# Kernel tuning notes

Measured on AMD Instinct MI355X. Metric: run time of the kernel, lower is better.

## Reference

```python
import jax, jax.numpy as jnp
import numpy as np

N = 4096      # nodes
F = 512       # nfeat
D = 64        # nhid per head
H = 8         # nheads
C = 40        # nclass
ALPHA = 0.2   # leakyrelu slope
NEG = -1e9    # mask value (finite for bf16/fp16 safety; exp -> 0)
EDGE_P = 0.004


def setup_inputs() -> dict:
    key = jax.random.key(0)
    ks = jax.random.split(key, 8)
    x = jax.random.normal(ks[0], (N, F), jnp.float32)
    adj = jax.random.uniform(ks[1], (N, N)) < EDGE_P
    adj = adj | jnp.eye(N, dtype=bool)  # self-loops: every softmax row valid
    init = lambda k, shape, fan: jax.random.normal(k, shape, jnp.float32) / np.sqrt(fan)
    W1 = init(ks[2], (H, F, D), F)        # per-head tran.weight^T
    a1_src = init(ks[3], (H, D), D)       # att1 (j / source term)
    a1_dst = init(ks[4], (H, D), D)       # att2 (i / destination term)
    W2 = init(ks[5], (H * D, C), H * D)   # output head tran
    a2_src = init(ks[6], (C,), C)
    a2_dst = init(ks[7], (C,), C)
    return dict(x=x, adj=adj, W1=W1, a1_src=a1_src, a1_dst=a1_dst,
                W2=W2, a2_src=a2_src, a2_dst=a2_dst)


def reference(x, adj, W1, a1_src, a1_dst, W2, a2_src, a2_dst):
    # ---- layer 1: H heads in parallel (dropout = identity in eval) ----
    h = jnp.einsum('nf,hfd->hnd', x, W1)              # [H,N,D]
    si = jnp.einsum('hnd,hd->hn', h, a1_dst)          # att2(h): i term
    sj = jnp.einsum('hnd,hd->hn', h, a1_src)          # att1(h): j term
    e = jax.nn.leaky_relu(si[:, :, None] + sj[:, None, :], ALPHA)  # [H,N,N]
    e = jnp.where(adj[None], e, NEG)                  # mask non-edges
    p = jax.nn.softmax(e, axis=-1)                    # softmax over neighbors j
    out = jnp.einsum('hij,hjd->hid', p, h)            # [H,N,D]
    # torch.cat(heads, dim=1) -> [N, H*D] with heads contiguous
    x2 = jax.nn.elu(jnp.transpose(out, (1, 0, 2)).reshape(N, H * D))
    # ---- output attention head ----
    h2 = x2 @ W2                                      # [N,C]
    e2 = jax.nn.leaky_relu((h2 @ a2_dst)[:, None] + (h2 @ a2_src)[None, :], ALPHA)
    e2 = jnp.where(adj, e2, NEG)
    p2 = jax.nn.softmax(e2, axis=-1)
    return p2 @ h2                                    # [N,C]
```

## Files before the change

### kernel.cpp

```cpp
#include <hip/hip_runtime.h>

#define NN 4096
#define FF 512
#define DD 64
#define HH 8
#define CC 40
#define HD (HH * DD)
#define CP 64
#define MAXDEG 128
#define ALPHA 0.2f

#define L2BM 8
#define L2BK 32

typedef __attribute__((ext_vector_type(8))) short bf16x8;
typedef __attribute__((ext_vector_type(4))) float f32x4;

__device__ __forceinline__ float bf2f(unsigned short u) {
    union { unsigned int i; float f; } v;
    v.i = ((unsigned int)u) << 16;
    return v.f;
}

__device__ __forceinline__ unsigned short f2bf(float f) {
    union { float f; unsigned int u; } v;
    v.f = f;
    unsigned int r = v.u + 0x7fffu + ((v.u >> 16) & 1u);
    return (unsigned short)(r >> 16);
}

__device__ __forceinline__ float wave_sum(float v) {
    #pragma unroll
    for (int off = 32; off; off >>= 1) v += __shfl_xor(v, off, 64);
    return v;
}

__device__ __forceinline__ float wave_max(float v) {
    #pragma unroll
    for (int off = 32; off; off >>= 1) v = fmaxf(v, __shfl_xor(v, off, 64));
    return v;
}

__device__ __forceinline__ float read_f(const void* src, int i, int isBf16) {
    if (isBf16) return bf2f(((const unsigned short*)src)[i]);
    return ((const float*)src)[i];
}

__device__ __forceinline__ int sniff_x(const void* xraw, int tid, int* fS) {
    if (tid == 0) *fS = 1;
    __syncthreads();
    int bad = 0;
    const unsigned int* xw = (const unsigned int*)xraw;
    #pragma unroll
    for (int q = 0; q < 4; q++) {
        unsigned int w = xw[(tid & 255) * 4 + q];
        unsigned int e0 = (w >> 7) & 0xffu;
        unsigned int e1 = (w >> 23) & 0xffu;
        if (e0 >= 0x90u || e1 >= 0x90u) bad = 1;
    }
    if (bad) *fS = 0;
    __syncthreads();
    return *fS;
}

__global__ __launch_bounds__(256) void prep(const unsigned char* __restrict__ adj,
                                            const void* __restrict__ x,
                                            const void* __restrict__ W1,
                                            const void* __restrict__ W2,
                                            const void* __restrict__ a1s,
                                            const void* __restrict__ a1d,
                                            const void* __restrict__ a2s,
                                            const void* __restrict__ a2d,
                                            int* __restrict__ nbr,
                                            int* __restrict__ deg,
                                            unsigned short* __restrict__ W1bth,
                                            unsigned short* __restrict__ W1btl,
                                            float* __restrict__ W2p,
                                            float* __restrict__ a1sf,
                                            float* __restrict__ a1df,
                                            float* __restrict__ a2sf,
                                            float* __restrict__ a2df) {
    __shared__ int cnt;
    __shared__ int fS;
    int t = threadIdx.x;
    int blk = blockIdx.x;

    if (blk < NN) {
        if (t == 0) { cnt = 0; fS = 1; }
        __syncthreads();
        if (adj[(size_t)t * (NN + 1)] == 0) fS = 0;
        __syncthreads();
        int isByte = fS;
        int i = blk;
        if (isByte) {
            uint4 v = ((const uint4*)(adj + (size_t)i * NN))[t];
            unsigned int u[4] = { v.x, v.y, v.z, v.w };
            int base = t * 16;
            #pragma unroll
            for (int q = 0; q < 4; q++) {
                #pragma unroll
                for (int b = 0; b < 4; b++) {
                    if ((u[q] >> (8 * b)) & 0xffu) {
                        int p = atomicAdd(&cnt, 1);
                        if (p < MAXDEG) nbr[(size_t)i * MAXDEG + p] = base + q * 4 + b;
                    }
                }
            }
        } else {
            const int4* row = (const int4*)((const int*)adj + (size_t)i * NN);
            #pragma unroll
            for (int q = 0; q < 4; q++) {
                int idx4 = q * 256 + t;
                int4 v = row[idx4];
                int base = idx4 * 4;
                if (v.x) { int p = atomicAdd(&cnt, 1); if (p < MAXDEG) nbr[(size_t)i * MAXDEG + p] = base; }
                if (v.y) { int p = atomicAdd(&cnt, 1); if (p < MAXDEG) nbr[(size_t)i * MAXDEG + p] = base + 1; }
                if (v.z) { int p = atomicAdd(&cnt, 1); if (p < MAXDEG) nbr[(size_t)i * MAXDEG + p] = base + 2; }
                if (v.w) { int p = atomicAdd(&cnt, 1); if (p < MAXDEG) nbr[(size_t)i * MAXDEG + p] = base + 3; }
            }
        }
        __syncthreads();
        if (t == 0) deg[i] = min(cnt, MAXDEG);
        return;
    }

    int bf = sniff_x(x, t, &fS);

    if (blk < NN + 64) {
        int b = blk - NN;
        int ob = b * 4096 + t * 16;
        int row = ob >> 9;
        int f0 = ob & 511;
        int hd = row >> 6, d = row & 63;
        unsigned short hi[16], lo[16];
        #pragma unroll
        for (int q = 0; q < 16; q++) {
            float v = read_f(W1, (hd * FF + f0 + q) * DD + d, bf);
            unsigned short h16 = f2bf(v);
            hi[q] = h16;
            lo[q] = f2bf(v - bf2f(h16));
        }
        #pragma unroll
        for (int q = 0; q < 16; q++) {
            W1bth[(size_t)row * FF + f0 + q] = hi[q];
            W1btl[(size_t)row * FF + f0 + q] = lo[q];
        }
        return;
    }

    int i = (blk - NN - 64) * 256 + t;
    const int nW2p = HD * CP;
    const int nA1 = HD;
    if (i < nW2p) {
        int k = i / CP, c = i % CP;
        W2p[i] = (c < CC) ? read_f(W2, k * CC + c, bf) : 0.f;
        return;
    }
    i -= nW2p;
    if (i < nA1) { a1sf[i] = read_f(a1s, i, bf); return; }
    i -= nA1;
    if (i < nA1) { a1df[i] = read_f(a1d, i, bf); return; }
    i -= nA1;
    if (i < CC) { a2sf[i] = read_f(a2s, i, bf); return; }
    i -= CC;
    if (i < CC) { a2df[i] = read_f(a2d, i, bf); return; }
}

__global__ __launch_bounds__(256) void l1_gemm(const void* __restrict__ xraw,
                                               const unsigned short* __restrict__ W1bth,
                                               const unsigned short* __restrict__ W1btl,
                                               const float* __restrict__ a1sf,
                                               const float* __restrict__ a1df,
                                               unsigned short* __restrict__ hb,
                                               float* __restrict__ siv,
                                               float* __restrict__ sjv) {
    __shared__ __align__(16) unsigned short AhB[2][64][40];
    __shared__ __align__(16) unsigned short BhB[2][64][40];
    __shared__ int fS;

    int bm = blockIdx.x, hd = blockIdx.y;
    int tid = threadIdx.x;
    int isBf16 = sniff_x(xraw, tid, &fS);

    int wave = tid >> 6, lane = tid & 63;
    int wm = wave >> 1, wn = wave & 1;
    int lr = lane & 15, lg = lane >> 4;
    int srow = tid >> 2;
    int sseg = (tid & 3) * 8;

    const unsigned short* wAp = W1bth + (size_t)(hd * 64 + srow) * FF + sseg;
    const unsigned short* wBp = W1btl + (size_t)(hd * 64 + srow) * FF + sseg;

    f32x4 acc[2][2];
    #pragma unroll
    for (int r = 0; r < 2; r++)
        #pragma unroll
        for (int c = 0; c < 2; c++) acc[r][c] = (f32x4){0.f, 0.f, 0.f, 0.f};

    if (isBf16) {
        const unsigned short* xp = (const unsigned short*)xraw
                                 + (size_t)(bm * 64 + srow) * FF + sseg;
        uint4 ra = *(const uint4*)xp;
        uint4 rb = *(const uint4*)wAp;
        #pragma unroll 4
        for (int kk = 0; kk < FF; kk += 32) {
            int p = (kk >> 5) & 1;
            *(uint4*)&AhB[p][srow][sseg] = ra;
            *(uint4*)&BhB[p][srow][sseg] = rb;
            __syncthreads();
            int kn = (kk + 32 < FF) ? kk + 32 : kk;
            ra = *(const uint4*)(xp + kn);
            rb = *(const uint4*)(wAp + kn);
            bf16x8 a0 = *(const bf16x8*)&AhB[p][wm * 32 + lr][lg * 8];
            bf16x8 a1 = *(const bf16x8*)&AhB[p][wm * 32 + 16 + lr][lg * 8];
            bf16x8 b0 = *(const bf16x8*)&BhB[p][wn * 32 + lr][lg * 8];
            bf16x8 b1 = *(const bf16x8*)&BhB[p][wn * 32 + 16 + lr][lg * 8];
            acc[0][0] = __builtin_amdgcn_mfma_f32_16x16x32_bf16(a0, b0, acc[0][0], 0, 0, 0);
            acc[0][1] = __builtin_amdgcn_mfma_f32_16x16x32_bf16(a0, b1, acc[0][1], 0, 0, 0);
            acc[1][0] = __builtin_amdgcn_mfma_f32_16x16x32_bf16(a1, b0, acc[1][0], 0, 0, 0);
            acc[1][1] = __builtin_amdgcn_mfma_f32_16x16x32_bf16(a1, b1, acc[1][1], 0, 0, 0);
        }
    } else {
        unsigned short (*Ah)[40] = AhB[0];
        unsigned short (*Al)[40] = AhB[1];
        unsigned short (*Bh)[40] = BhB[0];
        unsigned short (*Bl)[40] = BhB[1];
        const float* xp = (const float*)xraw + (size_t)(bm * 64 + srow) * FF + sseg;
        float4 ra0 = *(const float4*)xp;
        float4 ra1 = *(const float4*)(xp + 4);
        uint4 rbh = *(const uint4*)wAp;
        uint4 rbl = *(const uint4*)wBp;
        for (int kk = 0; kk < FF; kk += 32) {
            __syncthreads();
            union { unsigned short s[8]; uint4 v; } uh, ul;
            float fv[8] = { ra0.x, ra0.y, ra0.z, ra0.w, ra1.x, ra1.y, ra1.z, ra1.w };
            #pragma unroll
            for (int q = 0; q < 8; q++) {
                unsigned short h16 = f2bf(fv[q]);
                uh.s[q] = h16;
                ul.s[q] = f2bf(fv[q] - bf2f(h16));
            }
            *(uint4*)&Ah[srow][sseg] = uh.v;
            *(uint4*)&Al[srow][sseg] = ul.v;
            *(uint4*)&Bh[srow][sseg] = rbh;
            *(uint4*)&Bl[srow][sseg] = rbl;
            __syncthreads();
            int kn = (kk + 32 < FF) ? kk + 32 : kk;
            ra0 = *(const float4*)(xp + kn);
            ra1 = *(const float4*)(xp + kn + 4);
            rbh = *(const uint4*)(wAp + kn);
            rbl = *(const uint4*)(wBp + kn);

            bf16x8 a_h0 = *(const bf16x8*)&Ah[wm * 32 + lr][lg * 8];
            bf16x8 a_h1 = *(const bf16x8*)&Ah[wm * 32 + 16 + lr][lg * 8];
            bf16x8 a_l0 = *(const bf16x8*)&Al[wm * 32 + lr][lg * 8];
            bf16x8 a_l1 = *(const bf16x8*)&Al[wm * 32 + 16 + lr][lg * 8];
            bf16x8 b_h0 = *(const bf16x8*)&Bh[wn * 32 + lr][lg * 8];
            bf16x8 b_h1 = *(const bf16x8*)&Bh[wn * 32 + 16 + lr][lg * 8];
            bf16x8 b_l0 = *(const bf16x8*)&Bl[wn * 32 + lr][lg * 8];
            bf16x8 b_l1 = *(const bf16x8*)&Bl[wn * 32 + 16 + lr][lg * 8];

            acc[0][0] = __builtin_amdgcn_mfma_f32_16x16x32_bf16(a_h0, b_h0, acc[0][0], 0, 0, 0);
            acc[0][1] = __builtin_amdgcn_mfma_f32_16x16x32_bf16(a_h0, b_h1, acc[0][1], 0, 0, 0);
            acc[1][0] = __builtin_amdgcn_mfma_f32_16x16x32_bf16(a_h1, b_h0, acc[1][0], 0, 0, 0);
            acc[1][1] = __builtin_amdgcn_mfma_f32_16x16x32_bf16(a_h1, b_h1, acc[1][1], 0, 0, 0);
            acc[0][0] = __builtin_amdgcn_mfma_f32_16x16x32_bf16(a_h0, b_l0, acc[0][0], 0, 0, 0);
            acc[0][1] = __builtin_amdgcn_mfma_f32_16x16x32_bf16(a_h0, b_l1, acc[0][1], 0, 0, 0);
            acc[1][0] = __builtin_amdgcn_mfma_f32_16x16x32_bf16(a_h1, b_l0, acc[1][0], 0, 0, 0);
            acc[1][1] = __builtin_amdgcn_mfma_f32_16x16x32_bf16(a_h1, b_l1, acc[1][1], 0, 0, 0);
            acc[0][0] = __builtin_amdgcn_mfma_f32_16x16x32_bf16(a_l0, b_h0, acc[0][0], 0, 0, 0);
            acc[0][1] = __builtin_amdgcn_mfma_f32_16x16x32_bf16(a_l0, b_h1, acc[0][1], 0, 0, 0);
            acc[1][0] = __builtin_amdgcn_mfma_f32_16x16x32_bf16(a_l1, b_h0, acc[1][0], 0, 0, 0);
            acc[1][1] = __builtin_amdgcn_mfma_f32_16x16x32_bf16(a_l1, b_h1, acc[1][1], 0, 0, 0);
        }
    }

    float adv[2], asv[2];
    #pragma unroll
    for (int fc = 0; fc < 2; fc++) {
        adv[fc] = a1df[hd * DD + wn * 32 + fc * 16 + lr];
        asv[fc] = a1sf[hd * DD + wn * 32 + fc * 16 + lr];
    }
    float pdv[2][4], psv[2][4];
    #pragma unroll
    for (int fr = 0; fr < 2; fr++) {
        #pragma unroll
        for (int q = 0; q < 4; q++) {
            int row = bm * 64 + wm * 32 + fr * 16 + lg * 4 + q;
            int colb = hd * 64 + wn * 32;
            hb[(size_t)row * HD + colb + lr] = f2bf(acc[fr][0][q]);
            hb[(size_t)row * HD + colb + 16 + lr] = f2bf(acc[fr][1][q]);
            float pd = acc[fr][0][q] * adv[0] + acc[fr][1][q] * adv[1];
            float ps = acc[fr][0][q] * asv[0] + acc[fr][1][q] * asv[1];
            #pragma unroll
            for (int off = 1; off < 16; off <<= 1) {
                pd += __shfl_xor(pd, off, 64);
                ps += __shfl_xor(ps, off, 64);
            }
            pdv[fr][q] = pd;
            psv[fr][q] = ps;
        }
    }
    float* sred = (float*)&AhB[0][0][0];
    __syncthreads();
    if (wn == 0 && lr == 0) {
        #pragma unroll
        for (int fr = 0; fr < 2; fr++)
            #pragma unroll
            for (int q = 0; q < 4; q++) {
                int rl = wm * 32 + fr * 16 + lg * 4 + q;
                sred[rl * 2] = pdv[fr][q];
                sred[rl * 2 + 1] = psv[fr][q];
            }
    }
    __syncthreads();
    if (wn == 1 && lr == 0) {
        #pragma unroll
        for (int fr = 0; fr < 2; fr++)
            #pragma unroll
            for (int q = 0; q < 4; q++) {
                int rl = wm * 32 + fr * 16 + lg * 4 + q;
                int row = bm * 64 + rl;
                siv[(size_t)row * HH + hd] = sred[rl * 2] + pdv[fr][q];
                sjv[(size_t)row * HH + hd] = sred[rl * 2 + 1] + psv[fr][q];
            }
    }
}

__global__ __launch_bounds__(256) void l1_attn(const int* __restrict__ nbr,
                                               const int* __restrict__ deg,
                                               const unsigned short* __restrict__ hb,
                                               const float* __restrict__ siv,
                                               const float* __restrict__ sjv,
                                               float* __restrict__ x2) {
    int i = blockIdx.x;
    int tid = threadIdx.x;
    int wave = tid >> 6, lane = tid & 63;
    int d = deg[i];
    __shared__ int js[MAXDEG];
    __shared__ float wls[HH][MAXDEG];
    __shared__ float invs[HH];
    __shared__ __align__(16) float4 red[128];
    for (int k = tid; k < d; k += 256) js[k] = nbr[(size_t)i * MAXDEG + k];
    __syncthreads();

    int hd = wave * 2 + (lane >> 5);
    int l32 = lane & 31;
    float sii = siv[(size_t)i * HH + hd];
    float m = -1e30f;
    for (int k = l32; k < d; k += 32) {
        float sc = sii + sjv[(size_t)js[k] * HH + hd];
        sc = sc > 0.f ? sc : ALPHA * sc;
        wls[hd][k] = sc;
        m = fmaxf(m, sc);
    }
    #pragma unroll
    for (int off = 16; off; off >>= 1) m = fmaxf(m, __shfl_xor(m, off, 64));
    float s = 0.f;
    for (int k = l32; k < d; k += 32) {
        float e = expf(wls[hd][k] - m);
        wls[hd][k] = e;
        s += e;
    }
    #pragma unroll
    for (int off = 16; off; off >>= 1) s += __shfl_xor(s, off, 64);
    if (l32 == 0) invs[hd] = 1.f / fmaxf(s, 1e-30f);
    __syncthreads();

    const uint2* hu2 = (const uint2*)hb;
    int half = tid >> 7;
    int cq = tid & 127;
    const float* wl = wls[cq >> 4];
    float a0 = 0.f, a1 = 0.f, a2 = 0.f, a3 = 0.f;
    int kk = half;
    for (; kk + 4 <= d; kk += 4) {
        uint2 v0 = hu2[(size_t)js[kk] * 128 + cq];
        uint2 v1 = hu2[(size_t)js[kk + 2] * 128 + cq];
        float w0 = wl[kk], w1 = wl[kk + 2];
        a0 = fmaf(w0, bf2f((unsigned short)v0.x), a0);
        a1 = fmaf(w0, bf2f((unsigned short)(v0.x >> 16)), a1);
        a2 = fmaf(w0, bf2f((unsigned short)v0.y), a2);
        a3 = fmaf(w0, bf2f((unsigned short)(v0.y >> 16)), a3);
        a0 = fmaf(w1, bf2f((unsigned short)v1.x), a0);
        a1 = fmaf(w1, bf2f((unsigned short)(v1.x >> 16)), a1);
        a2 = fmaf(w1, bf2f((unsigned short)v1.y), a2);
        a3 = fmaf(w1, bf2f((unsigned short)(v1.y >> 16)), a3);
    }
    for (; kk < d; kk += 2) {
        uint2 v = hu2[(size_t)js[kk] * 128 + cq];
        float w = wl[kk];
        a0 = fmaf(w, bf2f((unsigned short)v.x), a0);
        a1 = fmaf(w, bf2f((unsigned short)(v.x >> 16)), a1);
        a2 = fmaf(w, bf2f((unsigned short)v.y), a2);
        a3 = fmaf(w, bf2f((unsigned short)(v.y >> 16)), a3);
    }
    if (half == 1) red[cq] = make_float4(a0, a1, a2, a3);
    __syncthreads();
    if (half == 0) {
        float4 r = red[cq];
        float inv = invs[cq >> 4];
        a0 = (a0 + r.x) * inv;
        a1 = (a1 + r.y) * inv;
        a2 = (a2 + r.z) * inv;
        a3 = (a3 + r.w) * inv;
        float4 o;
        o.x = a0 > 0.f ? a0 : expm1f(a0);
        o.y = a1 > 0.f ? a1 : expm1f(a1);
        o.z = a2 > 0.f ? a2 : expm1f(a2);
        o.w = a3 > 0.f ? a3 : expm1f(a3);
        *(float4*)(x2 + (size_t)i * HD + cq * 4) = o;
    }
}

__global__ __launch_bounds__(256) void l2_fused(const float* __restrict__ x2,
                                                const float* __restrict__ W2p,
                                                const float* __restrict__ a2sf,
                                                const float* __restrict__ a2df,
                                                float* __restrict__ h2,
                                                float* __restrict__ d1,
                                                float* __restrict__ d2) {
    __shared__ float As[L2BK][L2BM + 1];
    __shared__ float Bs[L2BK][CP + 1];
    int tid = threadIdx.x;
    int bm = blockIdx.x;
    int ar = tid >> 5;
    int ak = tid & 31;
    int br = tid >> 3;
    int bc = (tid & 7) * 8;
    int c = tid & 63;
    int r0 = (tid >> 6) * 2;

    const float* Arow = x2 + (size_t)(bm * L2BM + ar) * FF;

    float acc0 = 0.f, acc1 = 0.f;

    float av = Arow[ak];
    float4 bv0 = *(const float4*)(W2p + (size_t)br * CP + bc);
    float4 bv1 = *(const float4*)(W2p + (size_t)br * CP + bc + 4);

    for (int kk = 0; kk < FF; kk += L2BK) {
        __syncthreads();
        As[ak][ar] = av;
        *(float4*)&Bs[br][bc] = bv0;
        *(float4*)&Bs[br][bc + 4] = bv1;
        __syncthreads();
        int kn = (kk + L2BK < FF) ? kk + L2BK : kk;
        av = Arow[kn + ak];
        bv0 = *(const float4*)(W2p + (size_t)(kn + br) * CP + bc);
        bv1 = *(const float4*)(W2p + (size_t)(kn + br) * CP + bc + 4);
        #pragma unroll
        for (int k = 0; k < L2BK; k++) {
            float b = Bs[k][c];
            acc0 = fmaf(As[k][r0], b, acc0);
            acc1 = fmaf(As[k][r0 + 1], b, acc1);
        }
    }

    float accs[2] = { acc0, acc1 };
    float ad = (c < CC) ? a2df[c] : 0.f;
    float as = (c < CC) ? a2sf[c] : 0.f;
    #pragma unroll
    for (int q = 0; q < 2; q++) {
        int row = bm * L2BM + r0 + q;
        if (c < CC) h2[(size_t)row * CC + c] = accs[q];
        float pd = wave_sum(accs[q] * ad);
        float ps = wave_sum(accs[q] * as);
        if (c == 0) { d1[row] = pd; d2[row] = ps; }
    }
}

__global__ __launch_bounds__(256) void l2_attn(const int* __restrict__ nbr,
                                               const int* __restrict__ deg,
                                               const float* __restrict__ h2,
                                               const float* __restrict__ d1,
                                               const float* __restrict__ d2,
                                               float* __restrict__ out) {
    int w = threadIdx.x >> 6, lane = threadIdx.x & 63;
    int i = blockIdx.x * 4 + w;
    int d = deg[i];
    __shared__ int js[4][MAXDEG];
    __shared__ float wls[4][MAXDEG];
    for (int k = lane; k < d; k += 64) js[w][k] = nbr[(size_t)i * MAXDEG + k];

    float sii = d1[i];
    float m = -1e30f;
    for (int k = lane; k < d; k += 64) {
        float sc = sii + d2[js[w][k]];
        sc = sc > 0.f ? sc : ALPHA * sc;
        wls[w][k] = sc;
        m = fmaxf(m, sc);
    }
    m = wave_max(m);
    float s = 0.f;
    for (int k = lane; k < d; k += 64) {
        float e = expf(wls[w][k] - m);
        wls[w][k] = e;
        s += e;
    }
    s = fmaxf(wave_sum(s), 1e-30f);

    int c = lane;
    if (c < CC) {
        float acc = 0.f;
        int k = 0;
        for (; k + 4 <= d; k += 4) {
            float v0 = h2[(size_t)js[w][k] * CC + c];
            float v1 = h2[(size_t)js[w][k + 1] * CC + c];
            float v2 = h2[(size_t)js[w][k + 2] * CC + c];
            float v3 = h2[(size_t)js[w][k + 3] * CC + c];
            acc = fmaf(wls[w][k], v0, acc);
            acc = fmaf(wls[w][k + 1], v1, acc);
            acc = fmaf(wls[w][k + 2], v2, acc);
            acc = fmaf(wls[w][k + 3], v3, acc);
        }
        for (; k < d; k++)
            acc = fmaf(wls[w][k], h2[(size_t)js[w][k] * CC + c], acc);
        out[(size_t)i * CC + c] = acc / s;
    }
}

extern "C" void kernel_launch(void* const* d_in, const int* in_sizes, int n_in,
                              void* d_out, int out_size, void* d_ws, size_t ws_size,
                              hipStream_t stream) {
    const void* x   = d_in[0];
    const unsigned char* adj = (const unsigned char*)d_in[1];
    const void* W1  = d_in[2];
    const void* a1s = d_in[3];
    const void* a1d = d_in[4];
    const void* W2  = d_in[5];
    const void* a2s = d_in[6];
    const void* a2d = d_in[7];

    char* ws = (char*)d_ws;
    int*   nbr   = (int*)(ws + 0);
    int*   deg   = (int*)(ws + 2097152);
    float* siv   = (float*)(ws + 2113536);
    float* sjv   = (float*)(ws + 2244608);
    unsigned short* W1bth = (unsigned short*)(ws + 2375680);
    unsigned short* W1btl = (unsigned short*)(ws + 2899968);
    float* W2p   = (float*)(ws + 3424256);
    float* a1sf  = (float*)(ws + 3555328);
    float* a1df  = (float*)(ws + 3557376);
    float* a2sf  = (float*)(ws + 3559424);
    float* a2df  = (float*)(ws + 3559680);
    unsigned short* hb = (unsigned short*)(ws + 3559936);
    float* x2    = (float*)(ws + 7754240);
    float* h2    = (float*)(ws + 16142848);
    float* d1    = (float*)(ws + 16798208);
    float* d2    = (float*)(ws + 16814592);

    const int nSmall = HD * CP + 2 * HD + 2 * CC;
    const int prepGrid = NN + 64 + (nSmall + 255) / 256;

    hipLaunchKernelGGL(prep, dim3(prepGrid), dim3(256), 0, stream,
                       adj, x, W1, W2, a1s, a1d, a2s, a2d,
                       nbr, deg, W1bth, W1btl, W2p, a1sf, a1df, a2sf, a2df);
    hipLaunchKernelGGL(l1_gemm, dim3(NN / 64, HH), dim3(256), 0, stream,
                       x, W1bth, W1btl, a1sf, a1df, hb, siv, sjv);
    hipLaunchKernelGGL(l1_attn, dim3(NN), dim3(256), 0, stream,
                       nbr, deg, hb, siv, sjv, x2);
    hipLaunchKernelGGL(l2_fused, dim3(NN / L2BM), dim3(256), 0, stream,
                       x2, W2p, a2sf, a2df, h2, d1, d2);
    hipLaunchKernelGGL(l2_attn, dim3(NN / 4), dim3(256), 0, stream,
                       nbr, deg, h2, d1, d2, (float*)d_out);
}
```

Baseline: 171.1 us.

## Fuse four post-prep kernels into one persistent kernel with grid barriers

Replaces the separate layer-1 GEMM, layer-1 attention, layer-2 GEMM and layer-2 attention launches with a single persistent kernel of 1024 blocks. The blocks loop over work items and synchronise between stages through an atomic-counter grid barrier that prep resets. Shared memory for the four stages is overlaid in a union. This removes three kernel launch gaps and tail effects. In exchange it depends on all 1024 blocks being co-resident (launch_bounds 256,4), pays for spin-wait barriers, and may leave each stage with less parallelism than its own tuned grid had.

Result: slower. 493.3 us (+188.3%).

```diff
diff --git a/kernel.cpp b/kernel.cpp
--- a/kernel.cpp
+++ b/kernel.cpp
@@ -12,6 +12,7 @@
 
 #define L2BM 8
 #define L2BK 32
+#define MEGA_GRID 1024
 
 typedef __attribute__((ext_vector_type(8))) short bf16x8;
 typedef __attribute__((ext_vector_type(4))) float f32x4;
@@ -61,6 +62,17 @@
     if (bad) *fS = 0;
     __syncthreads();
     return *fS;
+}
+
+__device__ __forceinline__ void gbar(unsigned* bar, unsigned target) {
+    __syncthreads();
+    if (threadIdx.x == 0) {
+        __threadfence();
+        atomicAdd(bar, 1u);
+        while (atomicAdd(bar, 0u) < target) __builtin_amdgcn_s_sleep(16);
+        __threadfence();
+    }
+    __syncthreads();
 }
 
 __global__ __launch_bounds__(256) void prep(const unsigned char* __restrict__ adj,
@@ -79,11 +91,13 @@
                                             float* __restrict__ a1sf,
                                             float* __restrict__ a1df,
                                             float* __restrict__ a2sf,
-                                            float* __restrict__ a2df) {
+                                            float* __restrict__ a2df,
+                                            unsigned* __restrict__ bar) {
     __shared__ int cnt;
     __shared__ int fS;
     int t = threadIdx.x;
     int blk = blockIdx.x;
+    if (blk == 0 && t == 0) *bar = 0u;
 
     if (blk < NN) {
         if (t == 0) { cnt = 0; fS = 1; }
@@ -166,356 +180,350 @@
     if (i < CC) { a2df[i] = read_f(a2d, i, bf); return; }
 }
 
-__global__ __launch_bounds__(256) void l1_gemm(const void* __restrict__ xraw,
-                                               const unsigned short* __restrict__ W1bth,
-                                               const unsigned short* __restrict__ W1btl,
-                                               const float* __restrict__ a1sf,
-                                               const float* __restrict__ a1df,
-                                               unsigned short* __restrict__ hb,
-                                               float* __restrict__ siv,
-                                               float* __restrict__ sjv) {
-    __shared__ __align__(16) unsigned short AhB[2][64][40];
-    __shared__ __align__(16) unsigned short BhB[2][64][40];
+union __align__(16) SharedU {
+    struct { unsigned short Ah[64][40], Al[64][40], Bh[64][40], Bl[64][40]; } g1;
+    struct { int js[MAXDEG]; float wls[HH][MAXDEG]; float invs[HH]; float4 red[128]; } a1;
+    struct { float As[L2BK][L2BM + 1]; float Bs[L2BK][CP + 1]; } g2;
+    struct { int js[4][MAXDEG]; float wls[4][MAXDEG]; } a2;
+};
+
+__global__ __launch_bounds__(256, 4) void mega(
+        const void* __restrict__ xraw,
+        const unsigned short* __restrict__ W1bth,
+        const unsigned short* __restrict__ W1btl,
+        const float* __restrict__ a1sf,
+        const float* __restrict__ a1df,
+        const int* __restrict__ nbr,
+        const int* __restrict__ deg,
+        unsigned short* __restrict__ hb,
+        float* __restrict__ siv,
+        float* __restrict__ sjv,
+        float* __restrict__ x2,
+        const float* __restrict__ W2p,
+        const float* __restrict__ a2sf,
+        const float* __restrict__ a2df,
+        float* __restrict__ h2,
+        float* __restrict__ d1,
+        float* __restrict__ d2,
+        float* __restrict__ out,
+        unsigned* __restrict__ bar) {
+    __shared__ SharedU su;
     __shared__ int fS;
-
-    int bm = blockIdx.x, hd = blockIdx.y;
-    int tid = threadIdx.x;
+    const int tid = threadIdx.x;
+    const unsigned nb = gridDim.x;
+
     int isBf16 = sniff_x(xraw, tid, &fS);
 
-    int wave = tid >> 6, lane = tid & 63;
-    int wm = wave >> 1, wn = wave & 1;
-    int lr = lane & 15, lg = lane >> 4;
-    int srow = tid >> 2;
-    int sseg = (tid & 3) * 8;
-
-    const unsigned short* wAp = W1bth + (size_t)(hd * 64 + srow) * FF + sseg;
-    const unsigned short* wBp = W1btl + (size_t)(hd * 64 + srow) * FF + sseg;
-
-    f32x4 acc[2][2];
-    #pragma unroll
-    for (int r = 0; r < 2; r++)
-        #pragma unroll
-        for (int c = 0; c < 2; c++) acc[r][c] = (f32x4){0.f, 0.f, 0.f, 0.f};
-
-    if (isBf16) {
-        const unsigned short* xp = (const unsigned short*)xraw
-                                 + (size_t)(bm * 64 + srow) * FF + sseg;
-        uint4 ra = *(const uint4*)xp;
-        uint4 rb = *(const uint4*)wAp;
-        #pragma unroll 4
-        for (int kk = 0; kk < FF; kk += 32) {
-            int p = (kk >> 5) & 1;
-            *(uint4*)&AhB[p][srow][sseg] = ra;
-            *(uint4*)&BhB[p][srow][sseg] = rb;
-            __syncthreads();
-            int kn = (kk + 32 < FF) ? kk + 32 : kk;
-            ra = *(const uint4*)(xp + kn);
-            rb = *(const uint4*)(wAp + kn);
-            bf16x8 a0 = *(const bf16x8*)&AhB[p][wm * 32 + lr][lg * 8];
-            bf16x8 a1 = *(const bf16x8*)&AhB[p][wm * 32 + 16 + lr][lg * 8];
-            bf16x8 b0 = *(const bf16x8*)&BhB[p][wn * 32 + lr][lg * 8];
-            bf16x8 b1 = *(const bf16x8*)&BhB[p][wn * 32 + 16 + lr][lg * 8];
-            acc[0][0] = __builtin_amdgcn_mfma_f32_16x16x32_bf16(a0, b0, acc[0][0], 0, 0, 0);
-            acc[0][1] = __builtin_amdgcn_mfma_f32_16x16x32_bf16(a0, b1, acc[0][1], 0, 0, 0);
-            acc[1][0] = __builtin_amdgcn_mfma_f32_16x16x32_bf16(a1, b0, acc[1][0], 0, 0, 0);
-            acc[1][1] = __builtin_amdgcn_mfma_f32_16x16x32_bf16(a1, b1, acc[1][1], 0, 0, 0);
-        }
-    } else {
-        unsigned short (*Ah)[40] = AhB[0];
-        unsigned short (*Al)[40] = AhB[1];
-        unsigned short (*Bh)[40] = BhB[0];
-        unsigned short (*Bl)[40] = BhB[1];
-        const float* xp = (const float*)xraw + (size_t)(bm * 64 + srow) * FF + sseg;
-        float4 ra0 = *(const float4*)xp;
-        float4 ra1 = *(const float4*)(xp + 4);
-        uint4 rbh = *(const uint4*)wAp;
-        uint4 rbl = *(const uint4*)wBp;
-        for (int kk = 0; kk < FF; kk += 32) {
-            __syncthreads();
-            union { unsigned short s[8]; uint4 v; } uh, ul;
-            float fv[8] = { ra0.x, ra0.y, ra0.z, ra0.w, ra1.x, ra1.y, ra1.z, ra1.w };
-            #pragma unroll
-            for (int q = 0; q < 8; q++) {
-                unsigned short h16 = f2bf(fv[q]);
-                uh.s[q] = h16;
-                ul.s[q] = f2bf(fv[q] - bf2f(h16));
-            }
-            *(uint4*)&Ah[srow][sseg] = uh.v;
-            *(uint4*)&Al[srow][sseg] = ul.v;
-            *(uint4*)&Bh[srow][sseg] = rbh;
-            *(uint4*)&Bl[srow][sseg] = rbl;
-            __syncthreads();
-            int kn = (kk + 32 < FF) ? kk + 32 : kk;
-            ra0 = *(const float4*)(xp + kn);
-            ra1 = *(const float4*)(xp + kn + 4);
-            rbh = *(const uint4*)(wAp + kn);
-            rbl = *(const uint4*)(wBp + kn);
-
-            bf16x8 a_h0 = *(const bf16x8*)&Ah[wm * 32 + lr][lg * 8];
-            bf16x8 a_h1 = *(const bf16x8*)&Ah[wm * 32 + 16 + lr][lg * 8];
-            bf16x8 a_l0 = *(const bf16x8*)&Al[wm * 32 + lr][lg * 8];
-            bf16x8 a_l1 = *(const bf16x8*)&Al[wm * 32 + 16 + lr][lg * 8];
-            bf16x8 b_h0 = *(const bf16x8*)&Bh[wn * 32 + lr][lg * 8];
-            bf16x8 b_h1 = *(const bf16x8*)&Bh[wn * 32 + 16 + lr][lg * 8];
-            bf16x8 b_l0 = *(const bf16x8*)&Bl[wn * 32 + lr][lg * 8];
-            bf16x8 b_l1 = *(const bf16x8*)&Bl[wn * 32 + 16 + lr][lg * 8];
-
-            acc[0][0] = __builtin_amdgcn_mfma_f32_16x16x32_bf16(a_h0, b_h0, acc[0][0], 0, 0, 0);
-            acc[0][1] = __builtin_amdgcn_mfma_f32_16x16x32_bf16(a_h0, b_h1, acc[0][1], 0, 0, 0);
-            acc[1][0] = __builtin_amdgcn_mfma_f32_16x16x32_bf16(a_h1, b_h0, acc[1][0], 0, 0, 0);
-            acc[1][1] = __builtin_amdgcn_mfma_f32_16x16x32_bf16(a_h1, b_h1, acc[1][1], 0, 0, 0);
-            acc[0][0] = __builtin_amdgcn_mfma_f32_16x16x32_bf16(a_h0, b_l0, acc[0][0], 0, 0, 0);
-            acc[0][1] = __builtin_amdgcn_mfma_f32_16x16x32_bf16(a_h0, b_l1, acc[0][1], 0, 0, 0);
-            acc[1][0] = __builtin_amdgcn_mfma_f32_16x16x32_bf16(a_h1, b_l0, acc[1][0], 0, 0, 0);
-            acc[1][1] = __builtin_amdgcn_mfma_f32_16x16x32_bf16(a_h1, b_l1, acc[1][1], 0, 0, 0);
-            acc[0][0] = __builtin_amdgcn_mfma_f32_16x16x32_bf16(a_l0, b_h0, acc[0][0], 0, 0, 0);
-            acc[0][1] = __builtin_amdgcn_mfma_f32_16x16x32_bf16(a_l0, b_h1, acc[0][1], 0, 0, 0);
-            acc[1][0] = __builtin_amdgcn_mfma_f32_16x16x32_bf16(a_l1, b_h0, acc[1][0], 0, 0, 0);
-            acc[1][1] = __builtin_amdgcn_mfma_f32_16x16x32_bf16(a_l1, b_h1, acc[1][1], 0, 0, 0);
-        }
-    }
-
-    float adv[2], asv[2];
-    #pragma unroll
-    for (int fc = 0; fc < 2; fc++) {
-        adv[fc] = a1df[hd * DD + wn * 32 + fc * 16 + lr];
-        asv[fc] = a1sf[hd * DD + wn * 32 + fc * 16 + lr];
-    }
-    float pdv[2][4], psv[2][4];
-    #pragma unroll
-    for (int fr = 0; fr < 2; fr++) {
-        #pragma unroll
-        for (int q = 0; q < 4; q++) {
-            int row = bm * 64 + wm * 32 + fr * 16 + lg * 4 + q;
-            int colb = hd * 64 + wn * 32;
-            hb[(size_t)row * HD + colb + lr] = f2bf(acc[fr][0][q]);
-            hb[(size_t)row * HD + colb + 16 + lr] = f2bf(acc[fr][1][q]);
-            float pd = acc[fr][0][q] * adv[0] + acc[fr][1][q] * adv[1];
-            float ps = acc[fr][0][q] * asv[0] + acc[fr][1][q] * asv[1];
-            #pragma unroll
-            for (int off = 1; off < 16; off <<= 1) {
-                pd += __shfl_xor(pd, off, 64);
-                ps += __shfl_xor(ps, off, 64);
-            }
-            pdv[fr][q] = pd;
-            psv[fr][q] = ps;
-        }
-    }
-    float* sred = (float*)&AhB[0][0][0];
-    __syncthreads();
-    if (wn == 0 && lr == 0) {
-        #pragma unroll
-        for (int fr = 0; fr < 2; fr++)
-            #pragma unroll
-            for (int q = 0; q < 4; q++) {
-                int rl = wm * 32 + fr * 16 + lg * 4 + q;
-                sred[rl * 2] = pdv[fr][q];
-                sred[rl * 2 + 1] = psv[fr][q];
-            }
-    }
-    __syncthreads();
-    if (wn == 1 && lr == 0) {
-        #pragma unroll
-        for (int fr = 0; fr < 2; fr++)
-            #pragma unroll
-            for (int q = 0; q < 4; q++) {
-                int rl = wm * 32 + fr * 16 + lg * 4 + q;
-                int row = bm * 64 + rl;
-                siv[(size_t)row * HH + hd] = sred[rl * 2] + pdv[fr][q];
-                sjv[(size_t)row * HH + hd] = sred[rl * 2 + 1] + psv[fr][q];
-            }
-    }
-}
-
-__global__ __launch_bounds__(256) void l1_attn(const int* __restrict__ nbr,
-                                               const int* __restrict__ deg,
-                                               const unsigned short* __restrict__ hb,
-                                               const float* __restrict__ siv,
-                                               const float* __restrict__ sjv,
-                                               float* __restrict__ x2) {
-    int i = blockIdx.x;
-    int tid = threadIdx.x;
-    int wave = tid >> 6, lane = tid & 63;
-    int d = deg[i];
-    __shared__ int js[MAXDEG];
-    __shared__ float wls[HH][MAXDEG];
-    __shared__ float invs[HH];
-    __shared__ __align__(16) float4 red[128];
-    for (int k = tid; k < d; k += 256) js[k] = nbr[(size_t)i * MAXDEG + k];
-    __syncthreads();
-
-    int hd = wave * 2 + (lane >> 5);
-    int l32 = lane & 31;
-    float sii = siv[(size_t)i * HH + hd];
-    float m = -1e30f;
-    for (int k = l32; k < d; k += 32) {
-        float sc = sii + sjv[(size_t)js[k] * HH + hd];
-        sc = sc > 0.f ? sc : ALPHA * sc;
-        wls[hd][k] = sc;
-        m = fmaxf(m, sc);
-    }
-    #pragma unroll
-    for (int off = 16; off; off >>= 1) m = fmaxf(m, __shfl_xor(m, off, 64));
-    float s = 0.f;
-    for (int k = l32; k < d; k += 32) {
-        float e = expf(wls[hd][k] - m);
-        wls[hd][k] = e;
-        s += e;
-    }
-    #pragma unroll
-    for (int off = 16; off; off >>= 1) s += __shfl_xor(s, off, 64);
-    if (l32 == 0) invs[hd] = 1.f / fmaxf(s, 1e-30f);
-    __syncthreads();
-
-    const uint2* hu2 = (const uint2*)hb;
-    int half = tid >> 7;
-    int cq = tid & 127;
-    const float* wl = wls[cq >> 4];
-    float a0 = 0.f, a1 = 0.f, a2 = 0.f, a3 = 0.f;
-    int kk = half;
-    for (; kk + 4 <= d; kk += 4) {
-        uint2 v0 = hu2[(size_t)js[kk] * 128 + cq];
-        uint2 v1 = hu2[(size_t)js[kk + 2] * 128 + cq];
-        float w0 = wl[kk], w1 = wl[kk + 2];
-        a0 = fmaf(w0, bf2f((unsigned short)v0.x), a0);
-        a1 = fmaf(w0, bf2f((unsigned short)(v0.x >> 16)), a1);
-        a2 = fmaf(w0, bf2f((unsigned short)v0.y), a2);
-        a3 = fmaf(w0, bf2f((unsigned short)(v0.y >> 16)), a3);
-        a0 = fmaf(w1, bf2f((unsigned short)v1.x), a0);
-        a1 = fmaf(w1, bf2f((unsigned short)(v1.x >> 16)), a1);
-        a2 = fmaf(w1, bf2f((unsigned short)v1.y), a2);
-        a3 = fmaf(w1, bf2f((unsigned short)(v1.y >> 16)), a3);
-    }
-    for (; kk < d; kk += 2) {
-        uint2 v = hu2[(size_t)js[kk] * 128 + cq];
-        float w = wl[kk];
-        a0 = fmaf(w, bf2f((unsigned short)v.x), a0);
-        a1 = fmaf(w, bf2f((unsigned short)(v.x >> 16)), a1);
-        a2 = fmaf(w, bf2f((unsigned short)v.y), a2);
-        a3 = fmaf(w, bf2f((unsigned short)(v.y >> 16)), a3);
-    }
-    if (half == 1) red[cq] = make_float4(a0, a1, a2, a3);
-    __syncthreads();
-    if (half == 0) {
-        float4 r = red[cq];
-        float inv = invs[cq >> 4];
-        a0 = (a0 + r.x) * inv;
-        a1 = (a1 + r.y) * inv;
-        a2 = (a2 + r.z) * inv;
-        a3 = (a3 + r.w) * inv;
-        float4 o;
-        o.x = a0 > 0.f ? a0 : expm1f(a0);
-        o.y = a1 > 0.f ? a1 : expm1f(a1);
-        o.z = a2 > 0.f ? a2 : expm1f(a2);
-        o.w = a3 > 0.f ? a3 : expm1f(a3);
-        *(float4*)(x2 + (size_t)i * HD + cq * 4) = o;
-    }
-}
-
-__global__ __launch_bounds__(256) void l2_fused(const float* __restrict__ x2,
-                                                const float* __restrict__ W2p,
-                                                const float* __restrict__ a2sf,
-                                                const float* __restrict__ a2df,
-                                                float* __restrict__ h2,
-                                                float* __restrict__ d1,
-                                                float* __restrict__ d2) {
-    __shared__ float As[L2BK][L2BM + 1];
-    __shared__ float Bs[L2BK][CP + 1];
-    int tid = threadIdx.x;
-    int bm = blockIdx.x;
-    int ar = tid >> 5;
-    int ak = tid & 31;
-    int br = tid >> 3;
-    int bc = (tid & 7) * 8;
-    int c = tid & 63;
-    int r0 = (tid >> 6) * 2;
-
-    const float* Arow = x2 + (size_t)(bm * L2BM + ar) * FF;
-
-    float acc0 = 0.f, acc1 = 0.f;
-
-    float av = Arow[ak];
-    float4 bv0 = *(const float4*)(W2p + (size_t)br * CP + bc);
-    float4 bv1 = *(const float4*)(W2p + (size_t)br * CP + bc + 4);
-
-    for (int kk = 0; kk < FF; kk += L2BK) {
-        __syncthreads();
-        As[ak][ar] = av;
-        *(float4*)&Bs[br][bc] = bv0;
-        *(float4*)&Bs[br][bc + 4] = bv1;
-        __syncthreads();
-        int kn = (kk + L2BK < FF) ? kk + L2BK : kk;
-        av = Arow[kn + ak];
-        bv0 = *(const float4*)(W2p + (size_t)(kn + br) * CP + bc);
-        bv1 = *(const float4*)(W2p + (size_t)(kn + br) * CP + bc + 4);
-        #pragma unroll
-        for (int k = 0; k < L2BK; k++) {
-            float b = Bs[k][c];
-            acc0 = fmaf(As[k][r0], b, acc0);
-            acc1 = fmaf(As[k][r0 + 1], b, acc1);
-        }
-    }
-
-    float accs[2] = { acc0, acc1 };
-    float ad = (c < CC) ? a2df[c] : 0.f;
-    float as = (c < CC) ? a2sf[c] : 0.f;
-    #pragma unroll
-    for (int q = 0; q < 2; q++) {
-        int row = bm * L2BM + r0 + q;
-        if (c < CC) h2[(size_t)row * CC + c] = accs[q];
-        float pd = wave_sum(accs[q] * ad);
-        float ps = wave_sum(accs[q] * as);
-        if (c == 0) { d1[row] = pd; d2[row] = ps; }
-    }
-}
-
-__global__ __launch_bounds__(256) void l2_attn(const int* __restrict__ nbr,
-                                               const int* __restrict__ deg,
-                                               const float* __restrict__ h2,
-                                               const float* __restrict__ d1,
-                                               const float* __restrict__ d2,
-                                               float* __restrict__ out) {
-    int w = threadIdx.x >> 6, lane = threadIdx.x & 63;
-    int i = blockIdx.x * 4 + w;
-    int d = deg[i];
-    __shared__ int js[4][MAXDEG];
-    __shared__ float wls[4][MAXDEG];
-    for (int k = lane; k < d; k += 64) js[w][k] = nbr[(size_t)i * MAXDEG + k];
-
-    float sii = d1[i];
-    float m = -1e30f;
-    for (int k = lane; k < d; k += 64) {
-        float sc = sii + d2[js[w][k]];
-        sc = sc > 0.f ? sc : ALPHA * sc;
-        wls[w][k] = sc;
-        m = fmaxf(m, sc);
-    }
-    m = wave_max(m);
-    float s = 0.f;
-    for (int k = lane; k < d; k += 64) {
-        float e = expf(wls[w][k] - m);
-        wls[w][k] = e;
-        s += e;
-    }
-    s = fmaxf(wave_sum(s), 1e-30f);
-
-    int c = lane;
-    if (c < CC) {
-        float acc = 0.f;
-        int k = 0;
-        for (; k + 4 <= d; k += 4) {
-            float v0 = h2[(size_t)js[w][k] * CC + c];
-            float v1 = h2[(size_t)js[w][k + 1] * CC + c];
-            float v2 = h2[(size_t)js[w][k + 2] * CC + c];
-            float v3 = h2[(size_t)js[w][k + 3] * CC + c];
-            acc = fmaf(wls[w][k], v0, acc);
-            acc = fmaf(wls[w][k + 1], v1, acc);
-            acc = fmaf(wls[w][k + 2], v2, acc);
-            acc = fmaf(wls[w][k + 3], v3, acc);
-        }
-        for (; k < d; k++)
-            acc = fmaf(wls[w][k], h2[(size_t)js[w][k] * CC + c], acc);
-        out[(size_t)i * CC + c] = acc / s;
+    {
+        int wave = tid >> 6, lane = tid & 63;
+        int wm = wave >> 1, wn = wave & 1;
+        int lr = lane & 15, lg = lane >> 4;
+        int srow = tid >> 2, sseg = (tid & 3) * 8;
+
+        for (int tile = blockIdx.x; tile < (NN / 64) * HH; tile += nb) {
+            int bm = tile & 63, hd = tile >> 6;
+            const unsigned short* wAp = W1bth + (size_t)(hd * 64 + srow) * FF + sseg;
+            const unsigned short* wBp = W1btl + (size_t)(hd * 64 + srow) * FF + sseg;
+
+            f32x4 acc[2][2];
+            #pragma unroll
+            for (int r = 0; r < 2; r++)
+                #pragma unroll
+                for (int c = 0; c < 2; c++) acc[r][c] = (f32x4){0.f, 0.f, 0.f, 0.f};
+
+            if (isBf16) {
+                const unsigned short* xp = (const unsigned short*)xraw
+                                         + (size_t)(bm * 64 + srow) * FF + sseg;
+                uint4 ra = *(const uint4*)xp;
+                uint4 rb = *(const uint4*)wAp;
+                for (int kk = 0; kk < FF; kk += 32) {
+                    __syncthreads();
+                    *(uint4*)&su.g1.Ah[srow][sseg] = ra;
+                    *(uint4*)&su.g1.Bh[srow][sseg] = rb;
+                    __syncthreads();
+                    int kn = (kk + 32 < FF) ? kk + 32 : kk;
+                    ra = *(const uint4*)(xp + kn);
+                    rb = *(const uint4*)(wAp + kn);
+                    bf16x8 a0 = *(const bf16x8*)&su.g1.Ah[wm * 32 + lr][lg * 8];
+                    bf16x8 a1 = *(const bf16x8*)&su.g1.Ah[wm * 32 + 16 + lr][lg * 8];
+                    bf16x8 b0 = *(const bf16x8*)&su.g1.Bh[wn * 32 + lr][lg * 8];
+                    bf16x8 b1 = *(const bf16x8*)&su.g1.Bh[wn * 32 + 16 + lr][lg * 8];
+                    acc[0][0] = __builtin_amdgcn_mfma_f32_16x16x32_bf16(a0, b0, acc[0][0], 0, 0, 0);
+                    acc[0][1] = __builtin_amdgcn_mfma_f32_16x16x32_bf16(a0, b1, acc[0][1], 0, 0, 0);
+                    acc[1][0] = __builtin_amdgcn_mfma_f32_16x16x32_bf16(a1, b0, acc[1][0], 0, 0, 0);
+                    acc[1][1] = __builtin_amdgcn_mfma_f32_16x16x32_bf16(a1, b1, acc[1][1], 0, 0, 0);
+                }
+            } else {
+                const float* xp = (const float*)xraw + (size_t)(bm * 64 + srow) * FF + sseg;
+                float4 ra0 = *(const float4*)xp;
+                float4 ra1 = *(const float4*)(xp + 4);
+                uint4 rbh = *(const uint4*)wAp;
+                uint4 rbl = *(const uint4*)wBp;
+                for (int kk = 0; kk < FF; kk += 32) {
+                    __syncthreads();
+                    union { unsigned short s[8]; uint4 v; } uh, ul;
+                    float fv[8] = { ra0.x, ra0.y, ra0.z, ra0.w, ra1.x, ra1.y, ra1.z, ra1.w };
+                    #pragma unroll
+                    for (int q = 0; q < 8; q++) {
+                        unsigned short h16 = f2bf(fv[q]);
+                        uh.s[q] = h16;
+                        ul.s[q] = f2bf(fv[q] - bf2f(h16));
+                    }
+                    *(uint4*)&su.g1.Ah[srow][sseg] = uh.v;
+                    *(uint4*)&su.g1.Al[srow][sseg] = ul.v;
+                    *(uint4*)&su.g1.Bh[srow][sseg] = rbh;
+                    *(uint4*)&su.g1.Bl[srow][sseg] = rbl;
+                    __syncthreads();
+                    int kn = (kk + 32 < FF) ? kk + 32 : kk;
+                    ra0 = *(const float4*)(xp + kn);
+                    ra1 = *(const float4*)(xp + kn + 4);
+                    rbh = *(const uint4*)(wAp + kn);
+                    rbl = *(const uint4*)(wBp + kn);
+
+                    bf16x8 a_h0 = *(const bf16x8*)&su.g1.Ah[wm * 32 + lr][lg * 8];
+                    bf16x8 a_h1 = *(const bf16x8*)&su.g1.Ah[wm * 32 + 16 + lr][lg * 8];
+                    bf16x8 a_l0 = *(const bf16x8*)&su.g1.Al[wm * 32 + lr][lg * 8];
+                    bf16x8 a_l1 = *(const bf16x8*)&su.g1.Al[wm * 32 + 16 + lr][lg * 8];
+                    bf16x8 b_h0 = *(const bf16x8*)&su.g1.Bh[wn * 32 + lr][lg * 8];
+                    bf16x8 b_h1 = *(const bf16x8*)&su.g1.Bh[wn * 32 + 16 + lr][lg * 8];
+                    bf16x8 b_l0 = *(const bf16x8*)&su.g1.Bl[wn * 32 + lr][lg * 8];
+                    bf16x8 b_l1 = *(const bf16x8*)&su.g1.Bl[wn * 32 + 16 + lr][lg * 8];
+
+                    acc[0][0] = __builtin_amdgcn_mfma_f32_16x16x32_bf16(a_h0, b_h0, acc[0][0], 0, 0, 0);
+                    acc[0][1] = __builtin_amdgcn_mfma_f32_16x16x32_bf16(a_h0, b_h1, acc[0][1], 0, 0, 0);
+                    acc[1][0] = __builtin_amdgcn_mfma_f32_16x16x32_bf16(a_h1, b_h0, acc[1][0], 0, 0, 0);
+                    acc[1][1] = __builtin_amdgcn_mfma_f32_16x16x32_bf16(a_h1, b_h1, acc[1][1], 0, 0, 0);
+                    acc[0][0] = __builtin_amdgcn_mfma_f32_16x16x32_bf16(a_h0, b_l0, acc[0][0], 0, 0, 0);
+                    acc[0][1] = __builtin_amdgcn_mfma_f32_16x16x32_bf16(a_h0, b_l1, acc[0][1], 0, 0, 0);
+                    acc[1][0] = __builtin_amdgcn_mfma_f32_16x16x32_bf16(a_h1, b_l0, acc[1][0], 0, 0, 0);
+                    acc[1][1] = __builtin_amdgcn_mfma_f32_16x16x32_bf16(a_h1, b_l1, acc[1][1], 0, 0, 0);
+                    acc[0][0] = __builtin_amdgcn_mfma_f32_16x16x32_bf16(a_l0, b_h0, acc[0][0], 0, 0, 0);
+                    acc[0][1] = __builtin_amdgcn_mfma_f32_16x16x32_bf16(a_l0, b_h1, acc[0][1], 0, 0, 0);
+                    acc[1][0] = __builtin_amdgcn_mfma_f32_16x16x32_bf16(a_l1, b_h0, acc[1][0], 0, 0, 0);
+                    acc[1][1] = __builtin_amdgcn_mfma_f32_16x16x32_bf16(a_l1, b_h1, acc[1][1], 0, 0, 0);
+                }
+            }
+
+            float adv[2], asv[2];
+            #pragma unroll
+            for (int fc = 0; fc < 2; fc++) {
+                adv[fc] = a1df[hd * DD + wn * 32 + fc * 16 + lr];
+                asv[fc] = a1sf[hd * DD + wn * 32 + fc * 16 + lr];
+            }
+            float pdv[2][4], psv[2][4];
+            #pragma unroll
+            for (int fr = 0; fr < 2; fr++) {
+                #pragma unroll
+                for (int q = 0; q < 4; q++) {
+                    int row = bm * 64 + wm * 32 + fr * 16 + lg * 4 + q;
+                    int colb = hd * 64 + wn * 32;
+                    hb[(size_t)row * HD + colb + lr] = f2bf(acc[fr][0][q]);
+                    hb[(size_t)row * HD + colb + 16 + lr] = f2bf(acc[fr][1][q]);
+                    float pd = acc[fr][0][q] * adv[0] + acc[fr][1][q] * adv[1];
+                    float ps = acc[fr][0][q] * asv[0] + acc[fr][1][q] * asv[1];
+                    #pragma unroll
+                    for (int off = 1; off < 16; off <<= 1) {
+                        pd += __shfl_xor(pd, off, 64);
+                        ps += __shfl_xor(ps, off, 64);
+                    }
+                    pdv[fr][q] = pd;
+                    psv[fr][q] = ps;
+                }
+            }
+            float* sred = (float*)&su.g1.Ah[0][0];
+            __syncthreads();
+            if (wn == 0 && lr == 0) {
+                #pragma unroll
+                for (int fr = 0; fr < 2; fr++)
+                    #pragma unroll
+                    for (int q = 0; q < 4; q++) {
+                        int rl = wm * 32 + fr * 16 + lg * 4 + q;
+                        sred[rl * 2] = pdv[fr][q];
+                        sred[rl * 2 + 1] = psv[fr][q];
+                    }
+            }
+            __syncthreads();
+            if (wn == 1 && lr == 0) {
+                #pragma unroll
+                for (int fr = 0; fr < 2; fr++)
+                    #pragma unroll
+                    for (int q = 0; q < 4; q++) {
+                        int rl = wm * 32 + fr * 16 + lg * 4 + q;
+                        int row = bm * 64 + rl;
+                        siv[(size_t)row * HH + hd] = sred[rl * 2] + pdv[fr][q];
+                        sjv[(size_t)row * HH + hd] = sred[rl * 2 + 1] + psv[fr][q];
+                    }
+            }
+            __syncthreads();
+        }
+    }
+    gbar(bar, nb);
+
+    {
+        int wave = tid >> 6, lane = tid & 63;
+        int hd = wave * 2 + (lane >> 5);
+        int l32 = lane & 31;
+        int half = tid >> 7;
+        int cq = tid & 127;
+        for (int i = blockIdx.x; i < NN; i += nb) {
+            int d = deg[i];
+            for (int k = tid; k < d; k += 256) su.a1.js[k] = nbr[(size_t)i * MAXDEG + k];
+            __syncthreads();
+
+            float sii = siv[(size_t)i * HH + hd];
+            float m = -1e30f;
+            for (int k = l32; k < d; k += 32) {
+                float sc = sii + sjv[(size_t)su.a1.js[k] * HH + hd];
+                sc = sc > 0.f ? sc : ALPHA * sc;
+                su.a1.wls[hd][k] = sc;
+                m = fmaxf(m, sc);
+            }
+            #pragma unroll
+            for (int off = 16; off; off >>= 1) m = fmaxf(m, __shfl_xor(m, off, 64));
+            float s = 0.f;
+            for (int k = l32; k < d; k += 32) {
+                float e = expf(su.a1.wls[hd][k] - m);
+                su.a1.wls[hd][k] = e;
+                s += e;
+            }
+            #pragma unroll
+            for (int off = 16; off; off >>= 1) s += __shfl_xor(s, off, 64);
+            if (l32 == 0) su.a1.invs[hd] = 1.f / fmaxf(s, 1e-30f);
+            __syncthreads();
+
+            const uint2* hu2 = (const uint2*)hb;
+            const float* wl = su.a1.wls[cq >> 4];
+            float a0 = 0.f, a1 = 0.f, a2 = 0.f, a3 = 0.f;
+            int kk = half;
+            for (; kk + 4 <= d; kk += 4) {
+                uint2 v0 = hu2[(size_t)su.a1.js[kk] * 128 + cq];
+                uint2 v1 = hu2[(size_t)su.a1.js[kk + 2] * 128 + cq];
+                float w0 = wl[kk], w1 = wl[kk + 2];
+                a0 = fmaf(w0, bf2f((unsigned short)v0.x), a0);
+                a1 = fmaf(w0, bf2f((unsigned short)(v0.x >> 16)), a1);
+                a2 = fmaf(w0, bf2f((unsigned short)v0.y), a2);
+                a3 = fmaf(w0, bf2f((unsigned short)(v0.y >> 16)), a3);
+                a0 = fmaf(w1, bf2f((unsigned short)v1.x), a0);
+                a1 = fmaf(w1, bf2f((unsigned short)(v1.x >> 16)), a1);
+                a2 = fmaf(w1, bf2f((unsigned short)v1.y), a2);
+                a3 = fmaf(w1, bf2f((unsigned short)(v1.y >> 16)), a3);
+            }
+            for (; kk < d; kk += 2) {
+                uint2 v = hu2[(size_t)su.a1.js[kk] * 128 + cq];
+                float w = wl[kk];
+                a0 = fmaf(w, bf2f((unsigned short)v.x), a0);
+                a1 = fmaf(w, bf2f((unsigned short)(v.x >> 16)), a1);
+                a2 = fmaf(w, bf2f((unsigned short)v.y), a2);
+                a3 = fmaf(w, bf2f((unsigned short)(v.y >> 16)), a3);
+            }
+            if (half == 1) su.a1.red[cq] = make_float4(a0, a1, a2, a3);
+            __syncthreads();
+            if (half == 0) {
+                float4 r = su.a1.red[cq];
+                float inv = su.a1.invs[cq >> 4];
+                a0 = (a0 + r.x) * inv;
+                a1 = (a1 + r.y) * inv;
+                a2 = (a2 + r.z) * inv;
+                a3 = (a3 + r.w) * inv;
+                float4 o;
+                o.x = a0 > 0.f ? a0 : expm1f(a0);
+                o.y = a1 > 0.f ? a1 : expm1f(a1);
+                o.z = a2 > 0.f ? a2 : expm1f(a2);
+                o.w = a3 > 0.f ? a3 : expm1f(a3);
+                *(float4*)(x2 + (size_t)i * HD + cq * 4) = o;
+            }
+            __syncthreads();
+        }
+    }
+    gbar(bar, 2u * nb);
+
+    {
+        int ar = tid >> 5, ak = tid & 31;
+        int br = tid >> 3, bc = (tid & 7) * 8;
+        int c = tid & 63;
+        int r0 = (tid >> 6) * 2;
+        for (int bm = blockIdx.x; bm < NN / L2BM; bm += nb) {
+            const float* Arow = x2 + (size_t)(bm * L2BM + ar) * FF;
+            float acc0 = 0.f, acc1 = 0.f;
+            float av = Arow[ak];
+            float4 bv0 = *(const float4*)(W2p + (size_t)br * CP + bc);
+            float4 bv1 = *(const float4*)(W2p + (size_t)br * CP + bc + 4);
+            for (int kk = 0; kk < FF; kk += L2BK) {
+                __syncthreads();
+                su.g2.As[ak][ar] = av;
+                *(float4*)&su.g2.Bs[br][bc] = bv0;
+                *(float4*)&su.g2.Bs[br][bc + 4] = bv1;
+                __syncthreads();
+                int kn = (kk + L2BK < FF) ? kk + L2BK : kk;
+                av = Arow[kn + ak];
+                bv0 = *(const float4*)(W2p + (size_t)(kn + br) * CP + bc);
+                bv1 = *(const float4*)(W2p + (size_t)(kn + br) * CP + bc + 4);
+                #pragma unroll
+                for (int k = 0; k < L2BK; k++) {
+                    float b = su.g2.Bs[k][c];
+                    acc0 = fmaf(su.g2.As[k][r0], b, acc0);
+                    acc1 = fmaf(su.g2.As[k][r0 + 1], b, acc1);
+                }
+            }
+            float accs[2] = { acc0, acc1 };
+            float ad = (c < CC) ? a2df[c] : 0.f;
+            float as = (c < CC) ? a2sf[c] : 0.f;
+            #pragma unroll
+            for (int q = 0; q < 2; q++) {
+                int row = bm * L2BM + r0 + q;
+                if (c < CC) h2[(size_t)row * CC + c] = accs[q];
+                float pd = wave_sum(accs[q] * ad);
+                float ps = wave_sum(accs[q] * as);
+                if (c == 0) { d1[row] = pd; d2[row] = ps; }
+            }
+            __syncthreads();
+        }
+    }
+    gbar(bar, 3u * nb);
+
+    {
+        int w = tid >> 6, lane = tid & 63;
+        for (int g = blockIdx.x; g < NN / 4; g += nb) {
+            int i = g * 4 + w;
+            int d = deg[i];
+            for (int k = lane; k < d; k += 64) su.a2.js[w][k] = nbr[(size_t)i * MAXDEG + k];
+
+            float sii = d1[i];
+            float m = -1e30f;
+            for (int k = lane; k < d; k += 64) {
+                float sc = sii + d2[su.a2.js[w][k]];
+                sc = sc > 0.f ? sc : ALPHA * sc;
+                su.a2.wls[w][k] = sc;
+                m = fmaxf(m, sc);
+            }
+            m = wave_max(m);
+            float s = 0.f;
+            for (int k = lane; k < d; k += 64) {
+                float e = expf(su.a2.wls[w][k] - m);
+                su.a2.wls[w][k] = e;
+                s += e;
+            }
+            s = fmaxf(wave_sum(s), 1e-30f);
+
+            int c = lane;
+            if (c < CC) {
+                float acc = 0.f;
+                int k = 0;
+                for (; k + 4 <= d; k += 4) {
+                    float v0 = h2[(size_t)su.a2.js[w][k] * CC + c];
+                    float v1 = h2[(size_t)su.a2.js[w][k + 1] * CC + c];
+                    float v2 = h2[(size_t)su.a2.js[w][k + 2] * CC + c];
+                    float v3 = h2[(size_t)su.a2.js[w][k + 3] * CC + c];
+                    acc = fmaf(su.a2.wls[w][k], v0, acc);
+                    acc = fmaf(su.a2.wls[w][k + 1], v1, acc);
+                    acc = fmaf(su.a2.wls[w][k + 2], v2, acc);
+                    acc = fmaf(su.a2.wls[w][k + 3], v3, acc);
+                }
+                for (; k < d; k++)
+                    acc = fmaf(su.a2.wls[w][k], h2[(size_t)su.a2.js[w][k] * CC + c], acc);
+                out[(size_t)i * CC + c] = acc / s;
+            }
+        }
     }
 }
 
@@ -548,19 +556,16 @@
     float* h2    = (float*)(ws + 16142848);
     float* d1    = (float*)(ws + 16798208);
     float* d2    = (float*)(ws + 16814592);
+    unsigned* bar = (unsigned*)(ws + 16830976);
 
     const int nSmall = HD * CP + 2 * HD + 2 * CC;
     const int prepGrid = NN + 64 + (nSmall + 255) / 256;
 
     hipLaunchKernelGGL(prep, dim3(prepGrid), dim3(256), 0, stream,
                        adj, x, W1, W2, a1s, a1d, a2s, a2d,
-                       nbr, deg, W1bth, W1btl, W2p, a1sf, a1df, a2sf, a2df);
-    hipLaunchKernelGGL(l1_gemm, dim3(NN / 64, HH), dim3(256), 0, stream,
-                       x, W1bth, W1btl, a1sf, a1df, hb, siv, sjv);
-    hipLaunchKernelGGL(l1_attn, dim3(NN), dim3(256), 0, stream,
-                       nbr, deg, hb, siv, sjv, x2);
-    hipLaunchKernelGGL(l2_fused, dim3(NN / L2BM), dim3(256), 0, stream,
-                       x2, W2p, a2sf, a2df, h2, d1, d2);
-    hipLaunchKernelGGL(l2_attn, dim3(NN / 4), dim3(256), 0, stream,
-                       nbr, deg, h2, d1, d2, (float*)d_out);
-}
+                       nbr, deg, W1bth, W1btl, W2p, a1sf, a1df, a2sf, a2df, bar);
+    hipLaunchKernelGGL(mega, dim3(MEGA_GRID), dim3(256), 0, stream,
+                       x, W1bth, W1btl, a1sf, a1df, nbr, deg,
+                       hb, siv, sjv, x2, W2p, a2sf, a2df, h2, d1, d2,
+                       (float*)d_out, bar);
+}
```
